# Kernel optimization log

Measured on AMD Instinct MI355X. Metric: run time of the kernel, lower is better.

The kernel has to match this reference:

```python
import jax, jax.numpy as jnp
import numpy as np

MASK_FUTURE = True


def setup_inputs() -> dict:
    key = jax.random.key(0)
    kq, kk, kv = jax.random.split(key, 3)
    B, S, D = 4, 4096, 64
    query = jax.random.normal(kq, (B, S, D), dtype=jnp.float32)
    k = jax.random.normal(kk, (B, S, D), dtype=jnp.float32)
    value = jax.random.normal(kv, (B, S, D), dtype=jnp.float32)
    attention_mask = jnp.ones((B, S), dtype=jnp.int32)
    return {"query": query, "key": k, "value": value, "attention_mask": attention_mask}


def reference(query, key, value, attention_mask):
    B, Sq, D = query.shape
    Sk = key.shape[1]
    scale = 1.0 / jnp.sqrt(jnp.asarray(D, dtype=query.dtype))
    # [B, Sq, Sk] masked scaled scores
    scores = jnp.einsum("bqd,bkd->bqk", query, key) * scale
    valid = attention_mask[:, None, :] != 0  # padding mask, [B,1,Sk]
    if MASK_FUTURE and Sq == Sk:
        causal = jnp.arange(Sk)[None, :] <= jnp.arange(Sq)[:, None]  # [Sq,Sk]
        valid = valid & causal[None, :, :]
    scores = jnp.where(valid, scores, -jnp.inf)
    weights = jax.nn.softmax(scores, axis=-1)
    return jnp.einsum("bqk,bkd->bqd", weights, value)
```

## Files before the change

### kernel.cpp

```cpp
#include <hip/hip_runtime.h>
#include <hip/hip_bf16.h>

#define S_LEN 4096
#define DHEAD 64
#define KBLK 64
#define CSZ 8
#define NS 8
#define FM 12.0f

typedef __attribute__((ext_vector_type(8))) short bf16x8;
typedef __attribute__((ext_vector_type(8))) unsigned short u16x8;
typedef __attribute__((ext_vector_type(4))) float f32x4;

__device__ __forceinline__ unsigned short f2bf(float f) {
    union { float f; unsigned u; } v; v.f = f;
    unsigned r = v.u + 0x7fffu + ((v.u >> 16) & 1u);
    return (unsigned short)(r >> 16);
}

__device__ __forceinline__ float bf2f(unsigned short h) {
    union { unsigned u; float f; } v; v.u = ((unsigned)h) << 16; return v.f;
}

__device__ __forceinline__ unsigned pack_bf2(float a, float b) {
    __hip_bfloat162 h = __float22bfloat162_rn(float2{a, b});
    union { __hip_bfloat162 h; unsigned u; } cv; cv.h = h;
    return cv.u;
}

__device__ __forceinline__ float exp2_raw(float x) {
    float r;
    asm volatile("v_exp_f32 %0, %1\n\ts_nop 0" : "=v"(r) : "v"(x));
    return r;
}

__device__ __forceinline__ void gl_lds16(const void* g, void* l) {
    __builtin_amdgcn_global_load_lds(
        (const __attribute__((address_space(1))) void*)g,
        (__attribute__((address_space(3))) void*)l, 16, 0, 0);
}

__global__ __launch_bounds__(256) void prep(
        const float* __restrict__ K, const float* __restrict__ V,
        unsigned short* __restrict__ Kb, unsigned short* __restrict__ Vb)
{
    const int tile = blockIdx.x;
    const int b = tile >> 6, kt = tile & 63;
    const float* kp = K + ((size_t)(b * S_LEN + kt * KBLK)) * DHEAD;
    const float* vp = V + ((size_t)(b * S_LEN + kt * KBLK)) * DHEAD;
    unsigned short* kb = Kb + (size_t)tile * 4096;
    unsigned short* vb = Vb + (size_t)tile * 4096;
    const int tid = threadIdx.x;

    #pragma unroll
    for (int r = 0; r < 2; ++r) {
        int ci = r * 256 + tid;
        int base = ci * 16;
        int kr = base >> 7;
        int low = (base & 127) ^ ((kr & 7) << 4);
        int d0 = low >> 1;
        u16x8 o;
        #pragma unroll
        for (int j = 0; j < 8; ++j) o[j] = f2bf(kp[kr * DHEAD + d0 + j]);
        *(u16x8*)(kb + ci * 8) = o;
    }
    #pragma unroll
    for (int r = 0; r < 2; ++r) {
        int ci = r * 256 + tid;
        int base = ci * 16;
        int d = base >> 7;
        int low = (base & 127) ^ (((d >> 1) & 7) << 4);
        int slot0 = low >> 1;
        u16x8 o;
        #pragma unroll
        for (int j = 0; j < 8; ++j) {
            int slot = slot0 + j;
            int ct = 2 * ((slot >> 2) & 1) + ((slot >> 5) & 1);
            int k = ct * 16 + ((slot >> 3) & 3) * 4 + (slot & 3);
            o[j] = f2bf(vp[k * DHEAD + d]);
        }
        *(u16x8*)(vb + ci * 8) = o;
    }
}

__global__ __launch_bounds__(256) void attn_part(
        const float* __restrict__ Q, const unsigned short* __restrict__ Kb,
        const unsigned short* __restrict__ Vb, const int* __restrict__ mask,
        unsigned short* __restrict__ O_part, float* __restrict__ l_part, int Bn)
{
    __shared__ __align__(16) unsigned short K_lds[2][4096];
    __shared__ __align__(16) unsigned short V_lds[2][4096];
    __shared__ __align__(16) float mb[2][KBLK];

    const int blk = blockIdx.x;
    const int c   = blk & (NS - 1);
    const int bq  = 63 - ((blk >> 3) & 63);
    const int b   = blk >> 9;
    const int nt  = bq + 1;
    const int k0  = c * CSZ;
    if (k0 >= nt) return;
    const int k1  = (k0 + CSZ < nt) ? (k0 + CSZ) : nt;

    const int tid = threadIdx.x;
    const int lane = tid & 63;
    const int wq = tid >> 6;
    const int l15 = lane & 15;
    const int l4 = lane >> 4;
    const int q0 = bq * 64;
    const int qg = q0 + wq * 16 + l15;

    const float sc = 0.125f * 1.44269504088896340736f;

    bf16x8 qf[2];
    {
        const float* qp = Q + ((size_t)(b * S_LEN + qg)) * DHEAD + l4 * 8;
        for (int kk = 0; kk < 2; ++kk) {
            float4 a = *(const float4*)(qp + kk * 32);
            float4 cq = *(const float4*)(qp + kk * 32 + 4);
            bf16x8 f;
            f[0] = (short)f2bf(a.x * sc); f[1] = (short)f2bf(a.y * sc);
            f[2] = (short)f2bf(a.z * sc); f[3] = (short)f2bf(a.w * sc);
            f[4] = (short)f2bf(cq.x * sc); f[5] = (short)f2bf(cq.y * sc);
            f[6] = (short)f2bf(cq.z * sc); f[7] = (short)f2bf(cq.w * sc);
            qf[kk] = f;
        }
    }

    int mreg;
    auto STAGE = [&](int kt, int buf) {
        const unsigned short* kb = Kb + ((size_t)(b * 64 + kt)) * 4096;
        const unsigned short* vb = Vb + ((size_t)(b * 64 + kt)) * 4096;
        #pragma unroll
        for (int r = 0; r < 2; ++r) {
            int ci = r * 256 + tid;
            int ub = (r * 256 + wq * 64) * 16;
            gl_lds16(kb + ci * 8, (char*)&K_lds[buf][0] + ub);
            gl_lds16(vb + ci * 8, (char*)&V_lds[buf][0] + ub);
        }
        mreg = mask[(size_t)b * S_LEN + kt * KBLK + lane];
    };

    f32x4 acc[4];
    for (int t = 0; t < 4; ++t) acc[t] = (f32x4){0.f, 0.f, 0.f, 0.f};
    f32x4 lacc = (f32x4){0.f, 0.f, 0.f, 0.f};

    STAGE(k0, 0);
    if (tid < KBLK) mb[0][tid] = mreg ? -FM : -INFINITY;
    __syncthreads();
    int cur = 0;

    for (int kt = k0; kt < k1; ++kt) {
        const bool more = (kt + 1 < k1);
        if (more) STAGE(kt + 1, cur ^ 1);

        f32x4 s[4];
        __builtin_amdgcn_s_setprio(1);
        #pragma unroll
        for (int ct = 0; ct < 4; ++ct) {
            f32x4 z = (f32x4){0.f, 0.f, 0.f, 0.f};
            #pragma unroll
            for (int kk = 0; kk < 2; ++kk) {
                int row = ct * 16 + l15;
                int byte = (row * 128 + (l4 * 8 + kk * 32) * 2) ^ ((row & 7) << 4);
                bf16x8 kf = *(const bf16x8*)((const char*)&K_lds[cur][0] + byte);
                z = __builtin_amdgcn_mfma_f32_16x16x32_bf16(kf, qf[kk], z, 0, 0, 0);
            }
            s[ct] = z;
        }
        __builtin_amdgcn_s_setprio(0);

        const bool diag = (kt == nt - 1);
        f32x4 p[4];
        #pragma unroll
        for (int ct = 0; ct < 4; ++ct) {
            f32x4 bias4 = *(const f32x4*)&mb[cur][ct * 16 + l4 * 4];
            f32x4 v = s[ct] + bias4;
            if (diag) {
                int kb_ = kt * 64 + ct * 16 + l4 * 4;
                #pragma unroll
                for (int i = 0; i < 4; ++i)
                    if (kb_ + i > qg) v[i] = -INFINITY;
            }
            f32x4 pe;
            pe[0] = exp2_raw(v[0]); pe[1] = exp2_raw(v[1]);
            pe[2] = exp2_raw(v[2]); pe[3] = exp2_raw(v[3]);
            p[ct] = pe;
            lacc += pe;
        }

        bf16x8 pf[2];
        #pragma unroll
        for (int kk = 0; kk < 2; ++kk) {
            union { unsigned u[4]; bf16x8 v; } pk;
            pk.u[0] = pack_bf2(p[kk][0], p[kk][1]);
            pk.u[1] = pack_bf2(p[kk][2], p[kk][3]);
            pk.u[2] = pack_bf2(p[kk + 2][0], p[kk + 2][1]);
            pk.u[3] = pack_bf2(p[kk + 2][2], p[kk + 2][3]);
            pf[kk] = pk.v;
        }

        __builtin_amdgcn_s_setprio(1);
        #pragma unroll
        for (int kk = 0; kk < 2; ++kk) {
            #pragma unroll
            for (int t = 0; t < 4; ++t) {
                int d = t * 16 + l15;
                int vbyte = (d * 128 + (l4 * 8 + kk * 32) * 2) ^ (((d >> 1) & 7) << 4);
                bf16x8 vf = *(const bf16x8*)((const char*)&V_lds[cur][0] + vbyte);
                acc[t] = __builtin_amdgcn_mfma_f32_16x16x32_bf16(pf[kk], vf, acc[t], 0, 0, 0);
            }
        }
        __builtin_amdgcn_s_setprio(0);

        if (more && tid < KBLK) mb[cur ^ 1][tid] = mreg ? -FM : -INFINITY;
        __syncthreads();
        cur ^= 1;
    }

    float la = lacc[0] + lacc[1] + lacc[2] + lacc[3];
    la += __shfl_xor(la, 16);
    la += __shfl_xor(la, 32);

    for (int i = 0; i < 4; ++i) {
        int qr = q0 + wq * 16 + l4 * 4 + i;
        size_t rb = ((size_t)c * Bn + b) * S_LEN + qr;
        unsigned short* op = O_part + rb * 64 + l15;
        #pragma unroll
        for (int t = 0; t < 4; ++t)
            op[t * 16] = f2bf(acc[t][i]);
    }
    if (l4 == 0) {
        size_t rb = ((size_t)c * Bn + b) * S_LEN + qg;
        l_part[rb] = la;
    }
}

__global__ __launch_bounds__(256) void attn_reduce(
        const unsigned short* __restrict__ O_part, const float* __restrict__ l_part,
        float* __restrict__ out, int Bn)
{
    int g = blockIdx.x * 4 + (threadIdx.x >> 6);
    int d = threadIdx.x & 63;
    int b = g >> 12;
    int q = g & (S_LEN - 1);
    int nc = (q >> 9) + 1;

    float den = 0.f, acc = 0.f;
    for (int cc = 0; cc < nc; ++cc) {
        size_t rb = ((size_t)cc * Bn + b) * S_LEN + q;
        den += l_part[rb];
        acc += bf2f(O_part[rb * 64 + d]);
    }
    out[((size_t)b * S_LEN + q) * 64 + d] = acc / den;
}

__global__ __launch_bounds__(256) void attn_fwd(
        const float* __restrict__ Q, const float* __restrict__ K,
        const float* __restrict__ V, const int* __restrict__ mask,
        float* __restrict__ out)
{
    __shared__ __align__(16) unsigned short K_lds[KBLK * DHEAD];
    __shared__ __align__(16) unsigned short Vt_lds[DHEAD * KBLK];
    __shared__ __align__(16) unsigned short P_lds[4 * 16 * KBLK];
    __shared__ float mb[KBLK];

    const int tid = threadIdx.x;
    const int lane = tid & 63;
    const int wq = tid >> 6;
    const int l15 = lane & 15;
    const int l4 = lane >> 4;

    const int bq = blockIdx.x & 63;
    const int b  = blockIdx.x >> 6;
    const int q0 = bq * 64;
    const int nt = bq + 1;

    const float sc = 0.125f * 1.44269504088896340736f;

    bf16x8 qf[2];
    {
        const float* qp = Q + ((size_t)(b * S_LEN + q0 + wq * 16 + l15)) * DHEAD + l4 * 8;
        for (int kk = 0; kk < 2; ++kk) {
            float4 a = *(const float4*)(qp + kk * 32);
            float4 c = *(const float4*)(qp + kk * 32 + 4);
            bf16x8 f;
            f[0] = (short)f2bf(a.x * sc); f[1] = (short)f2bf(a.y * sc);
            f[2] = (short)f2bf(a.z * sc); f[3] = (short)f2bf(a.w * sc);
            f[4] = (short)f2bf(c.x * sc); f[5] = (short)f2bf(c.y * sc);
            f[6] = (short)f2bf(c.z * sc); f[7] = (short)f2bf(c.w * sc);
            qf[kk] = f;
        }
    }

    float4 kv[4];
    float4 vv[4];
    int    mreg;
    const int rp_  = (tid >> 4) << 1;
    const int d4v_ = (tid & 15) << 2;

    auto LOAD_TILE = [&](int kt) {
        const float* kp = K + ((size_t)(b * S_LEN + kt * KBLK)) * DHEAD;
        #pragma unroll
        for (int r = 0; r < 4; ++r) {
            int qi = tid + 256 * r;
            int kr = qi >> 4, d4 = (qi & 15) << 2;
            kv[r] = *(const float4*)(kp + kr * DHEAD + d4);
        }
        const float* vp = V + ((size_t)(b * S_LEN + kt * KBLK)) * DHEAD;
        #pragma unroll
        for (int r = 0; r < 2; ++r) {
            int row0 = rp_ + r * 32;
            vv[2 * r]     = *(const float4*)(vp + row0 * DHEAD + d4v_);
            vv[2 * r + 1] = *(const float4*)(vp + (row0 + 1) * DHEAD + d4v_);
        }
        mreg = mask[(size_t)b * S_LEN + kt * KBLK + (tid & 63)];
    };

    auto WRITE_TILE = [&]() {
        #pragma unroll
        for (int r = 0; r < 4; ++r) {
            int qi = tid + 256 * r;
            int kr = qi >> 4, d4 = (qi & 15) << 2;
            float4 v = kv[r];
            uint2 h;
            h.x = pack_bf2(v.x, v.y);
            h.y = pack_bf2(v.z, v.w);
            int byte = (kr * 128 + d4 * 2) ^ ((kr & 7) << 4);
            *(uint2*)((char*)K_lds + byte) = h;
        }
        #pragma unroll
        for (int r = 0; r < 2; ++r) {
            int row0 = rp_ + r * 32;
            float4 a = vv[2 * r];
            float4 c = vv[2 * r + 1];
            #pragma unroll
            for (int j = 0; j < 4; ++j) {
                int d = d4v_ + j;
                float aj = (j == 0) ? a.x : (j == 1) ? a.y : (j == 2) ? a.z : a.w;
                float cj = (j == 0) ? c.x : (j == 1) ? c.y : (j == 2) ? c.z : c.w;
                unsigned pack = pack_bf2(aj, cj);
                int byte = (d * 128 + row0 * 2) ^ ((d & 7) << 4);
                *(unsigned*)((char*)Vt_lds + byte) = pack;
            }
        }
        if (tid < KBLK)
            mb[tid] = mreg ? -FM : -INFINITY;
    };

    f32x4 acc[4];
    for (int t = 0; t < 4; ++t) acc[t] = (f32x4){0.f, 0.f, 0.f, 0.f};
    float l_acc[4] = {0.f, 0.f, 0.f, 0.f};

    LOAD_TILE(0);

    for (int kt = 0; kt < nt; ++kt) {
        __syncthreads();
        WRITE_TILE();
        __syncthreads();
        if (kt + 1 < nt) LOAD_TILE(kt + 1);

        f32x4 s[4];
        for (int ct = 0; ct < 4; ++ct) {
            f32x4 z = (f32x4){0.f, 0.f, 0.f, 0.f};
            for (int kk = 0; kk < 2; ++kk) {
                int row = ct * 16 + l15;
                int byte = (row * 128 + (l4 * 8 + kk * 32) * 2) ^ ((row & 7) << 4);
                bf16x8 kf = *(const bf16x8*)((const char*)K_lds + byte);
                z = __builtin_amdgcn_mfma_f32_16x16x32_bf16(qf[kk], kf, z, 0, 0, 0);
            }
            s[ct] = z;
        }

        const bool diag = (kt == nt - 1);
        for (int ct = 0; ct < 4; ++ct) {
            float bias = mb[ct * 16 + l15];
            int colg = kt * KBLK + ct * 16 + l15;
            for (int i = 0; i < 4; ++i) {
                float v = s[ct][i] + bias;
                if (diag) {
                    int qg2 = q0 + wq * 16 + l4 * 4 + i;
                    if (colg > qg2) v = -INFINITY;
                }
                float p = exp2_raw(v);
                l_acc[i] += p;
                int row = l4 * 4 + i;
                int col = ct * 16 + l15;
                int byte = (row * 128 + col * 2) ^ ((row & 7) << 4);
                *(unsigned short*)((char*)P_lds + wq * 2048 + byte) = f2bf(p);
            }
        }

        for (int kk = 0; kk < 2; ++kk) {
            int pbyte = (l15 * 128 + (l4 * 8 + kk * 32) * 2) ^ ((l15 & 7) << 4);
            bf16x8 pf = *(const bf16x8*)((const char*)P_lds + wq * 2048 + pbyte);
            for (int t = 0; t < 4; ++t) {
                int d = t * 16 + l15;
                int vbyte = (d * 128 + (l4 * 8 + kk * 32) * 2) ^ ((d & 7) << 4);
                bf16x8 vf = *(const bf16x8*)((const char*)Vt_lds + vbyte);
                acc[t] = __builtin_amdgcn_mfma_f32_16x16x32_bf16(pf, vf, acc[t], 0, 0, 0);
            }
        }
    }

    for (int i = 0; i < 4; ++i) {
        float v = l_acc[i];
        v += __shfl_xor(v, 1);
        v += __shfl_xor(v, 2);
        v += __shfl_xor(v, 4);
        v += __shfl_xor(v, 8);
        l_acc[i] = v;
    }

    for (int i = 0; i < 4; ++i) {
        float inv = 1.0f / l_acc[i];
        int qg2 = q0 + wq * 16 + l4 * 4 + i;
        float* op = out + ((size_t)(b * S_LEN + qg2)) * DHEAD + l15;
        for (int t = 0; t < 4; ++t)
            op[t * 16] = acc[t][i] * inv;
    }
}

extern "C" void kernel_launch(void* const* d_in, const int* in_sizes, int n_in,
                              void* d_out, int out_size, void* d_ws, size_t ws_size,
                              hipStream_t stream) {
    const float* Q = (const float*)d_in[0];
    const float* K = (const float*)d_in[1];
    const float* V = (const float*)d_in[2];
    const int* mask = (const int*)d_in[3];
    float* out = (float*)d_out;
    int Bn = in_sizes[0] / (S_LEN * DHEAD);

    size_t oN = (size_t)NS * Bn * S_LEN * 64;
    size_t lN = (size_t)NS * Bn * S_LEN;
    size_t bN = (size_t)Bn * 64 * 4096;
    size_t need = oN * 2 + lN * 4 + bN * 2 * 2;
    if (ws_size >= need) {
        unsigned short* O_part = (unsigned short*)d_ws;
        float* l_part = (float*)(O_part + oN);
        unsigned short* Kb = (unsigned short*)(l_part + lN);
        unsigned short* Vb = Kb + bN;
        prep<<<dim3(Bn * 64), dim3(256), 0, stream>>>(K, V, Kb, Vb);
        attn_part<<<dim3(Bn * 64 * NS), dim3(256), 0, stream>>>(
            Q, Kb, Vb, mask, O_part, l_part, Bn);
        attn_reduce<<<dim3(Bn * S_LEN / 4), dim3(256), 0, stream>>>(
            O_part, l_part, out, Bn);
    } else {
        attn_fwd<<<dim3(Bn * 64), dim3(256), 0, stream>>>(Q, K, V, mask, out);
    }
}
```

Baseline: 50.74 us.

## Load pre-swizzled K/V fragments directly into registers, drop LDS staging

The prep kernel now writes K and V tiles in MFMA-fragment order into one interleaved buffer, and precomputes the mask bias per tile. The attention kernel becomes a single-wavefront block per 16-query tile that loads its K/V fragments straight from global memory into registers, with no LDS, double buffering or barriers. This removes shared-memory staging and synchronisation, but each wave now rereads the whole K/V tile from cache with no sharing across waves and no explicit prefetch overlap. There are also four times more blocks, each shorter.

```diff
diff --git a/kernel.cpp b/kernel.cpp
--- a/kernel.cpp
+++ b/kernel.cpp
@@ -34,86 +34,73 @@
     return r;
 }
 
-__device__ __forceinline__ void gl_lds16(const void* g, void* l) {
-    __builtin_amdgcn_global_load_lds(
-        (const __attribute__((address_space(1))) void*)g,
-        (__attribute__((address_space(3))) void*)l, 16, 0, 0);
-}
-
 __global__ __launch_bounds__(256) void prep(
         const float* __restrict__ K, const float* __restrict__ V,
-        unsigned short* __restrict__ Kb, unsigned short* __restrict__ Vb)
+        const int* __restrict__ mask,
+        unsigned short* __restrict__ Tb, float* __restrict__ Mb)
 {
     const int tile = blockIdx.x;
     const int b = tile >> 6, kt = tile & 63;
     const float* kp = K + ((size_t)(b * S_LEN + kt * KBLK)) * DHEAD;
     const float* vp = V + ((size_t)(b * S_LEN + kt * KBLK)) * DHEAD;
-    unsigned short* kb = Kb + (size_t)tile * 4096;
-    unsigned short* vb = Vb + (size_t)tile * 4096;
+    unsigned short* tb = Tb + (size_t)tile * 8192;
     const int tid = threadIdx.x;
 
     #pragma unroll
-    for (int r = 0; r < 2; ++r) {
-        int ci = r * 256 + tid;
-        int base = ci * 16;
-        int kr = base >> 7;
-        int low = (base & 127) ^ ((kr & 7) << 4);
-        int d0 = low >> 1;
+    for (int r = 0; r < 4; ++r) {
+        int c16 = r * 256 + tid;
+        int lane = c16 & 63, f = (c16 >> 6) & 7, half = c16 >> 9;
+        int l15 = lane & 15, l4 = lane >> 4;
         u16x8 o;
-        #pragma unroll
-        for (int j = 0; j < 8; ++j) o[j] = f2bf(kp[kr * DHEAD + d0 + j]);
-        *(u16x8*)(kb + ci * 8) = o;
-    }
-    #pragma unroll
-    for (int r = 0; r < 2; ++r) {
-        int ci = r * 256 + tid;
-        int base = ci * 16;
-        int d = base >> 7;
-        int low = (base & 127) ^ (((d >> 1) & 7) << 4);
-        int slot0 = low >> 1;
-        u16x8 o;
-        #pragma unroll
-        for (int j = 0; j < 8; ++j) {
-            int slot = slot0 + j;
-            int ct = 2 * ((slot >> 2) & 1) + ((slot >> 5) & 1);
-            int k = ct * 16 + ((slot >> 3) & 3) * 4 + (slot & 3);
-            o[j] = f2bf(vp[k * DHEAD + d]);
-        }
-        *(u16x8*)(vb + ci * 8) = o;
-    }
-}
-
-__global__ __launch_bounds__(256) void attn_part(
-        const float* __restrict__ Q, const unsigned short* __restrict__ Kb,
-        const unsigned short* __restrict__ Vb, const int* __restrict__ mask,
+        if (half == 0) {
+            int ct = f >> 1, kk = f & 1;
+            const float* src = kp + (ct * 16 + l15) * DHEAD + kk * 32 + l4 * 8;
+            float4 a = *(const float4*)src;
+            float4 c2 = *(const float4*)(src + 4);
+            o[0] = f2bf(a.x); o[1] = f2bf(a.y); o[2] = f2bf(a.z); o[3] = f2bf(a.w);
+            o[4] = f2bf(c2.x); o[5] = f2bf(c2.y); o[6] = f2bf(c2.z); o[7] = f2bf(c2.w);
+        } else {
+            int t = f >> 1, kk = f & 1;
+            int d = t * 16 + l15;
+            #pragma unroll
+            for (int j = 0; j < 8; ++j) {
+                int k = (2 * ((j >> 2) & 1) + kk) * 16 + l4 * 4 + (j & 3);
+                o[j] = f2bf(vp[k * DHEAD + d]);
+            }
+        }
+        *(u16x8*)(tb + c16 * 8) = o;
+    }
+    if (tid < KBLK)
+        Mb[(size_t)tile * 64 + tid] =
+            mask[(size_t)b * S_LEN + kt * KBLK + tid] ? -FM : -INFINITY;
+}
+
+__global__ __launch_bounds__(64, 3) void attn_part(
+        const float* __restrict__ Q, const unsigned short* __restrict__ Tb,
+        const float* __restrict__ Mb,
         unsigned short* __restrict__ O_part, float* __restrict__ l_part, int Bn)
 {
-    __shared__ __align__(16) unsigned short K_lds[2][4096];
-    __shared__ __align__(16) unsigned short V_lds[2][4096];
-    __shared__ __align__(16) float mb[2][KBLK];
-
     const int blk = blockIdx.x;
     const int c   = blk & (NS - 1);
-    const int bq  = 63 - ((blk >> 3) & 63);
-    const int b   = blk >> 9;
-    const int nt  = bq + 1;
+    const int qt  = 255 - ((blk >> 3) & 255);
+    const int b   = blk >> 11;
+    const int q0  = qt * 16;
+    const int nt  = (q0 >> 6) + 1;
     const int k0  = c * CSZ;
     if (k0 >= nt) return;
     const int k1  = (k0 + CSZ < nt) ? (k0 + CSZ) : nt;
 
-    const int tid = threadIdx.x;
-    const int lane = tid & 63;
-    const int wq = tid >> 6;
+    const int lane = threadIdx.x;
     const int l15 = lane & 15;
     const int l4 = lane >> 4;
-    const int q0 = bq * 64;
-    const int qg = q0 + wq * 16 + l15;
+    const int qg = q0 + l15;
 
     const float sc = 0.125f * 1.44269504088896340736f;
 
     bf16x8 qf[2];
     {
         const float* qp = Q + ((size_t)(b * S_LEN + qg)) * DHEAD + l4 * 8;
+        #pragma unroll
         for (int kk = 0; kk < 2; ++kk) {
             float4 a = *(const float4*)(qp + kk * 32);
             float4 cq = *(const float4*)(qp + kk * 32 + 4);
@@ -126,45 +113,34 @@
         }
     }
 
-    int mreg;
-    auto STAGE = [&](int kt, int buf) {
-        const unsigned short* kb = Kb + ((size_t)(b * 64 + kt)) * 4096;
-        const unsigned short* vb = Vb + ((size_t)(b * 64 + kt)) * 4096;
-        #pragma unroll
-        for (int r = 0; r < 2; ++r) {
-            int ci = r * 256 + tid;
-            int ub = (r * 256 + wq * 64) * 16;
-            gl_lds16(kb + ci * 8, (char*)&K_lds[buf][0] + ub);
-            gl_lds16(vb + ci * 8, (char*)&V_lds[buf][0] + ub);
-        }
-        mreg = mask[(size_t)b * S_LEN + kt * KBLK + lane];
-    };
-
     f32x4 acc[4];
+    #pragma unroll
     for (int t = 0; t < 4; ++t) acc[t] = (f32x4){0.f, 0.f, 0.f, 0.f};
     f32x4 lacc = (f32x4){0.f, 0.f, 0.f, 0.f};
 
-    STAGE(k0, 0);
-    if (tid < KBLK) mb[0][tid] = mreg ? -FM : -INFINITY;
-    __syncthreads();
-    int cur = 0;
-
-    for (int kt = k0; kt < k1; ++kt) {
-        const bool more = (kt + 1 < k1);
-        if (more) STAGE(kt + 1, cur ^ 1);
+    const unsigned short* tb = Tb + ((size_t)(b * 64 + k0)) * 8192 + lane * 8;
+    const float* mbp = Mb + ((size_t)(b * 64 + k0)) * 64 + l4 * 4;
+
+    for (int kt = k0; kt < k1; ++kt, tb += 8192, mbp += 64) {
+        bf16x8 kfr[8], vfr[8];
+        #pragma unroll
+        for (int f = 0; f < 8; ++f)
+            kfr[f] = *(const bf16x8*)(tb + f * 512);
+        #pragma unroll
+        for (int f = 0; f < 8; ++f)
+            vfr[f] = *(const bf16x8*)(tb + 4096 + f * 512);
+        f32x4 bias[4];
+        #pragma unroll
+        for (int ct = 0; ct < 4; ++ct)
+            bias[ct] = *(const f32x4*)(mbp + ct * 16);
 
         f32x4 s[4];
         __builtin_amdgcn_s_setprio(1);
         #pragma unroll
         for (int ct = 0; ct < 4; ++ct) {
             f32x4 z = (f32x4){0.f, 0.f, 0.f, 0.f};
-            #pragma unroll
-            for (int kk = 0; kk < 2; ++kk) {
-                int row = ct * 16 + l15;
-                int byte = (row * 128 + (l4 * 8 + kk * 32) * 2) ^ ((row & 7) << 4);
-                bf16x8 kf = *(const bf16x8*)((const char*)&K_lds[cur][0] + byte);
-                z = __builtin_amdgcn_mfma_f32_16x16x32_bf16(kf, qf[kk], z, 0, 0, 0);
-            }
+            z = __builtin_amdgcn_mfma_f32_16x16x32_bf16(kfr[ct * 2 + 0], qf[0], z, 0, 0, 0);
+            z = __builtin_amdgcn_mfma_f32_16x16x32_bf16(kfr[ct * 2 + 1], qf[1], z, 0, 0, 0);
             s[ct] = z;
         }
         __builtin_amdgcn_s_setprio(0);
@@ -173,8 +149,7 @@
         f32x4 p[4];
         #pragma unroll
         for (int ct = 0; ct < 4; ++ct) {
-            f32x4 bias4 = *(const f32x4*)&mb[cur][ct * 16 + l4 * 4];
-            f32x4 v = s[ct] + bias4;
+            f32x4 v = s[ct] + bias[ct];
             if (diag) {
                 int kb_ = kt * 64 + ct * 16 + l4 * 4;
                 #pragma unroll
@@ -203,26 +178,20 @@
         #pragma unroll
         for (int kk = 0; kk < 2; ++kk) {
             #pragma unroll
-            for (int t = 0; t < 4; ++t) {
-                int d = t * 16 + l15;
-                int vbyte = (d * 128 + (l4 * 8 + kk * 32) * 2) ^ (((d >> 1) & 7) << 4);
-                bf16x8 vf = *(const bf16x8*)((const char*)&V_lds[cur][0] + vbyte);
-                acc[t] = __builtin_amdgcn_mfma_f32_16x16x32_bf16(pf[kk], vf, acc[t], 0, 0, 0);
-            }
+            for (int t = 0; t < 4; ++t)
+                acc[t] = __builtin_amdgcn_mfma_f32_16x16x32_bf16(
+                    pf[kk], vfr[t * 2 + kk], acc[t], 0, 0, 0);
         }
         __builtin_amdgcn_s_setprio(0);
-
-        if (more && tid < KBLK) mb[cur ^ 1][tid] = mreg ? -FM : -INFINITY;
-        __syncthreads();
-        cur ^= 1;
     }
 
     float la = lacc[0] + lacc[1] + lacc[2] + lacc[3];
     la += __shfl_xor(la, 16);
     la += __shfl_xor(la, 32);
 
+    #pragma unroll
     for (int i = 0; i < 4; ++i) {
-        int qr = q0 + wq * 16 + l4 * 4 + i;
+        int qr = q0 + l4 * 4 + i;
         size_t rb = ((size_t)c * Bn + b) * S_LEN + qr;
         unsigned short* op = O_part + rb * 64 + l15;
         #pragma unroll
@@ -432,16 +401,17 @@
 
     size_t oN = (size_t)NS * Bn * S_LEN * 64;
     size_t lN = (size_t)NS * Bn * S_LEN;
-    size_t bN = (size_t)Bn * 64 * 4096;
-    size_t need = oN * 2 + lN * 4 + bN * 2 * 2;
+    size_t tN = (size_t)Bn * 64 * 8192;
+    size_t mN = (size_t)Bn * 64 * 64;
+    size_t need = oN * 2 + lN * 4 + tN * 2 + mN * 4;
     if (ws_size >= need) {
         unsigned short* O_part = (unsigned short*)d_ws;
         float* l_part = (float*)(O_part + oN);
-        unsigned short* Kb = (unsigned short*)(l_part + lN);
-        unsigned short* Vb = Kb + bN;
-        prep<<<dim3(Bn * 64), dim3(256), 0, stream>>>(K, V, Kb, Vb);
-        attn_part<<<dim3(Bn * 64 * NS), dim3(256), 0, stream>>>(
-            Q, Kb, Vb, mask, O_part, l_part, Bn);
+        unsigned short* Tb = (unsigned short*)(l_part + lN);
+        float* Mb = (float*)(Tb + tN);
+        prep<<<dim3(Bn * 64), dim3(256), 0, stream>>>(K, V, mask, Tb, Mb);
+        attn_part<<<dim3(Bn * 256 * NS), dim3(64), 0, stream>>>(
+            Q, Tb, Mb, O_part, l_part, Bn);
         attn_reduce<<<dim3(Bn * S_LEN / 4), dim3(256), 0, stream>>>(
             O_part, l_part, out, Bn);
     } else {
```

New measurement: 60.44 us. +19.1%, slower.
